# Optimization experiments

Hardware: AMD Instinct MI355X
Metric: run time of the kernel (lower is better)

## Reference

```python
import jax, jax.numpy as jnp
import numpy as np

B, SPLIT, D = 4096, 32, 256
UNITS = 256  # must equal D for the final view in the original module


def setup_inputs() -> dict:
    key = jax.random.key(0)
    kx, kw, kb = jax.random.split(key, 3)
    x = jax.random.normal(kx, (B, SPLIT, D), dtype=jnp.float32)
    W = jax.random.normal(kw, (SPLIT, D, UNITS), dtype=jnp.float32) * 0.02
    b = jax.random.normal(kb, (SPLIT, UNITS), dtype=jnp.float32) * 0.02
    return {"x": x, "W": W, "b": b}


def reference(x, W, b):
    # Original: loop over split dim, per-split matmul + bias + activation, concat,
    # then view(B, split, input_dim). Fused here as a single batched einsum.
    out = jnp.einsum('bsd,sdu->bsu', x, W) + b[None, :, :]
    out = jax.nn.relu(out)  # activation
    # concat along dim 1 then view(B, split, input_dim) == [B, SPLIT, UNITS] since UNITS == D
    return out
```

## Files before the change

### kernel.cpp

```cpp
#include <hip/hip_runtime.h>
#include <hip/hip_bf16.h>

typedef __attribute__((ext_vector_type(8))) short bf16x8;
typedef __attribute__((ext_vector_type(4))) float f32x4;

#define SPLITN 32
#define DDIM   256
#define UNITS  256
#define BROWS  4096

#define NIT  16
#define MCHN (BROWS / (NIT * 16))

static __device__ __forceinline__ ushort f2bf(float f) {
    __hip_bfloat16 h = __float2bfloat16(f);
    return *reinterpret_cast<ushort*>(&h);
}

static __device__ __forceinline__ bf16x8 cvt8(f32x4 lo, f32x4 hi) {
    union { uint u32[4]; bf16x8 v; } r;
    r.u32[0] = (uint)f2bf(lo[0]) | ((uint)f2bf(lo[1]) << 16);
    r.u32[1] = (uint)f2bf(lo[2]) | ((uint)f2bf(lo[3]) << 16);
    r.u32[2] = (uint)f2bf(hi[0]) | ((uint)f2bf(hi[1]) << 16);
    r.u32[3] = (uint)f2bf(hi[2]) | ((uint)f2bf(hi[3]) << 16);
    return r.v;
}

__global__ __launch_bounds__(256) void wt_prep(const float* __restrict__ W,
                                               ushort* __restrict__ Wt) {
    __shared__ float tile[64][65];
    const int s  = blockIdx.z;
    const int d0 = blockIdx.y * 64;
    const int u0 = blockIdx.x * 64;
    const int t  = threadIdx.x;

    const float* Ws = W + s * 65536;
    #pragma unroll
    for (int i = 0; i < 4; ++i) {
        int f  = t + i * 256;
        int d  = f >> 4;
        int uq = f & 15;
        f32x4 v = *reinterpret_cast<const f32x4*>(Ws + (d0 + d) * 256 + u0 + uq * 4);
        tile[d][uq * 4 + 0] = v[0];
        tile[d][uq * 4 + 1] = v[1];
        tile[d][uq * 4 + 2] = v[2];
        tile[d][uq * 4 + 3] = v[3];
    }
    __syncthreads();

    ushort* Wts = Wt + s * 65536;
    #pragma unroll
    for (int i = 0; i < 4; ++i) {
        int g  = t + i * 256;
        int u  = g >> 4;
        int dq = g & 15;
        uint lo = (uint)f2bf(tile[dq * 4 + 0][u]) | ((uint)f2bf(tile[dq * 4 + 1][u]) << 16);
        uint hi = (uint)f2bf(tile[dq * 4 + 2][u]) | ((uint)f2bf(tile[dq * 4 + 3][u]) << 16);
        uint2 val; val.x = lo; val.y = hi;
        *reinterpret_cast<uint2*>(Wts + (u0 + u) * 256 + d0 + dq * 4) = val;
    }
}

__global__ __launch_bounds__(256, 2) void lc_gemm(const float* __restrict__ x,
                                                  const ushort* __restrict__ Wt,
                                                  const float* __restrict__ bias,
                                                  float* __restrict__ out) {
    const int bid = blockIdx.x;
    const int sw  = (bid & 7) * 64 + (bid >> 3);
    const int s   = sw >> 4;
    const int mc  = sw & 15;
    const int m0  = mc * (NIT * 16);

    const int t  = threadIdx.x;
    const int wc = t >> 6;
    const int l  = t & 63;
    const int lr = l & 15;
    const int lg = l >> 4;

    bf16x8 Bf[4][8];
    {
        const ushort* wb = Wt + s * 65536 + (wc * 64 + lr) * 256 + lg * 8;
        #pragma unroll
        for (int ni = 0; ni < 4; ++ni)
            #pragma unroll
            for (int k = 0; k < 8; ++k)
                Bf[ni][k] = *reinterpret_cast<const bf16x8*>(wb + ni * (16 * 256) + k * 32);
    }

    float bv[4];
    #pragma unroll
    for (int ni = 0; ni < 4; ++ni)
        bv[ni] = bias[s * 256 + wc * 64 + ni * 16 + lr];

    const float* xp = x + (long)(m0 + lr) * 8192 + s * 256 + lg * 8;

    f32x4 a[8][2];
    #pragma unroll
    for (int k = 0; k < 8; ++k) {
        a[k][0] = *reinterpret_cast<const f32x4*>(xp + k * 32);
        a[k][1] = *reinterpret_cast<const f32x4*>(xp + k * 32 + 4);
    }

    float* op = out + (long)(m0 + lg * 4) * 8192 + s * 256 + wc * 64 + lr;

    for (int it = 0; it < NIT; ++it) {
        const int nit = (it + 1 < NIT) ? (it + 1) : it;
        const float* xn = xp + (long)nit * (16 * 8192);

        f32x4 acc[4];
        #pragma unroll
        for (int ni = 0; ni < 4; ++ni) {
            f32x4 z = {0.f, 0.f, 0.f, 0.f};
            acc[ni] = z;
        }

        #pragma unroll
        for (int k = 0; k < 8; ++k) {
            bf16x8 af = cvt8(a[k][0], a[k][1]);
            f32x4 n0 = *reinterpret_cast<const f32x4*>(xn + k * 32);
            f32x4 n1 = *reinterpret_cast<const f32x4*>(xn + k * 32 + 4);
            #pragma unroll
            for (int ni = 0; ni < 4; ++ni)
                acc[ni] = __builtin_amdgcn_mfma_f32_16x16x32_bf16(
                    af, Bf[ni][k], acc[ni], 0, 0, 0);
            a[k][0] = n0;
            a[k][1] = n1;
        }

        #pragma unroll
        for (int ni = 0; ni < 4; ++ni) {
            #pragma unroll
            for (int rr = 0; rr < 4; ++rr) {
                float v = fmaxf(acc[ni][rr] + bv[ni], 0.f);
                __builtin_nontemporal_store(
                    v, op + (long)(it * 16 + rr) * 8192 + ni * 16);
            }
        }
    }
}

__global__ void naive_lc(const float* __restrict__ x, const float* __restrict__ W,
                         const float* __restrict__ b, float* __restrict__ out,
                         int total) {
    int i = blockIdx.x * blockDim.x + threadIdx.x;
    if (i >= total) return;
    int u = i & 255;
    int s = (i >> 8) & 31;
    int bi = i >> 13;
    const float* xr = x + (long)bi * 8192 + s * 256;
    const float* wc = W + s * 65536 + u;
    float acc = 0.f;
    #pragma unroll 4
    for (int d = 0; d < 256; ++d) acc += xr[d] * wc[d * 256];
    out[i] = fmaxf(acc + b[s * 256 + u], 0.f);
}

extern "C" void kernel_launch(void* const* d_in, const int* in_sizes, int n_in,
                              void* d_out, int out_size, void* d_ws, size_t ws_size,
                              hipStream_t stream) {
    const float* x = (const float*)d_in[0];
    const float* W = (const float*)d_in[1];
    const float* b = (const float*)d_in[2];
    float* out = (float*)d_out;

    const size_t wt_bytes = (size_t)SPLITN * DDIM * UNITS * sizeof(ushort);
    if (ws_size >= wt_bytes) {
        ushort* Wt = (ushort*)d_ws;
        wt_prep<<<dim3(4, 4, 32), 256, 0, stream>>>(W, Wt);
        lc_gemm<<<dim3(SPLITN * MCHN), 256, 0, stream>>>(x, Wt, b, out);
    } else {
        int total = BROWS * SPLITN * UNITS;
        naive_lc<<<(total + 255) / 256, 256, 0, stream>>>(x, W, b, out, total);
    }
}
```

Baseline: 270.1 us.

## Swap operand residency: keep x fragments in registers, stream weights per column chunk

```diff
diff --git a/kernel.cpp b/kernel.cpp
--- a/kernel.cpp
+++ b/kernel.cpp
@@ -8,9 +8,6 @@
 #define DDIM   256
 #define UNITS  256
 #define BROWS  4096
-
-#define NIT  16
-#define MCHN (BROWS / (NIT * 16))
 
 static __device__ __forceinline__ ushort f2bf(float f) {
     __hip_bfloat16 h = __float2bfloat16(f);
@@ -61,51 +58,38 @@
     }
 }
 
-__global__ __launch_bounds__(256, 2) void lc_gemm(const float* __restrict__ x,
+__global__ __launch_bounds__(256, 5) void lc_gemm(const float* __restrict__ x,
                                                   const ushort* __restrict__ Wt,
                                                   const float* __restrict__ bias,
                                                   float* __restrict__ out) {
     const int bid = blockIdx.x;
-    const int sw  = (bid & 7) * 64 + (bid >> 3);
-    const int s   = sw >> 4;
-    const int mc  = sw & 15;
-    const int m0  = mc * (NIT * 16);
+    const int sw  = (bid & 7) * 256 + (bid >> 3);
+    const int s   = sw >> 6;
+    const int rc  = sw & 63;
+    const int t   = threadIdx.x;
+    const int w   = t >> 6, l = t & 63;
+    const int lr  = l & 15, lg = l >> 4;
+    const int m0  = rc * 64 + w * 16;
 
-    const int t  = threadIdx.x;
-    const int wc = t >> 6;
-    const int l  = t & 63;
-    const int lr = l & 15;
-    const int lg = l >> 4;
-
-    bf16x8 Bf[4][8];
-    {
-        const ushort* wb = Wt + s * 65536 + (wc * 64 + lr) * 256 + lg * 8;
-        #pragma unroll
-        for (int ni = 0; ni < 4; ++ni)
-            #pragma unroll
-            for (int k = 0; k < 8; ++k)
-                Bf[ni][k] = *reinterpret_cast<const bf16x8*>(wb + ni * (16 * 256) + k * 32);
+    const float* xp = x + (long)(m0 + lr) * 8192 + s * 256 + lg * 8;
+    bf16x8 Af[8];
+    #pragma unroll
+    for (int k = 0; k < 8; ++k) {
+        f32x4 lo = *reinterpret_cast<const f32x4*>(xp + k * 32);
+        f32x4 hi = *reinterpret_cast<const f32x4*>(xp + k * 32 + 4);
+        Af[k] = cvt8(lo, hi);
     }
 
-    float bv[4];
-    #pragma unroll
-    for (int ni = 0; ni < 4; ++ni)
-        bv[ni] = bias[s * 256 + wc * 64 + ni * 16 + lr];
+    const ushort* wb = Wt + s * 65536 + lr * 256 + lg * 8;
+    const float*  bb = bias + s * 256 + lr;
+    float*        ob = out + (long)(m0 + lg * 4) * 8192 + s * 256 + lr;
 
-    const float* xp = x + (long)(m0 + lr) * 8192 + s * 256 + lg * 8;
+    for (int c = 0; c < 4; ++c) {
+        const ushort* wbc = wb + c * (64 * 256);
 
-    f32x4 a[8][2];
-    #pragma unroll
-    for (int k = 0; k < 8; ++k) {
-        a[k][0] = *reinterpret_cast<const f32x4*>(xp + k * 32);
-        a[k][1] = *reinterpret_cast<const f32x4*>(xp + k * 32 + 4);
-    }
-
-    float* op = out + (long)(m0 + lg * 4) * 8192 + s * 256 + wc * 64 + lr;
-
-    for (int it = 0; it < NIT; ++it) {
-        const int nit = (it + 1 < NIT) ? (it + 1) : it;
-        const float* xn = xp + (long)nit * (16 * 8192);
+        float bv[4];
+        #pragma unroll
+        for (int ni = 0; ni < 4; ++ni) bv[ni] = bb[c * 64 + ni * 16];
 
         f32x4 acc[4];
         #pragma unroll
@@ -114,28 +98,38 @@
             acc[ni] = z;
         }
 
+        bf16x8 B0[4], B1[4];
         #pragma unroll
-        for (int k = 0; k < 8; ++k) {
-            bf16x8 af = cvt8(a[k][0], a[k][1]);
-            f32x4 n0 = *reinterpret_cast<const f32x4*>(xn + k * 32);
-            f32x4 n1 = *reinterpret_cast<const f32x4*>(xn + k * 32 + 4);
+        for (int ni = 0; ni < 4; ++ni)
+            B0[ni] = *reinterpret_cast<const bf16x8*>(wbc + ni * (16 * 256));
+
+        #pragma unroll
+        for (int k = 0; k < 8; k += 2) {
+            #pragma unroll
+            for (int ni = 0; ni < 4; ++ni)
+                B1[ni] = *reinterpret_cast<const bf16x8*>(wbc + ni * (16 * 256) + (k + 1) * 32);
             #pragma unroll
             for (int ni = 0; ni < 4; ++ni)
                 acc[ni] = __builtin_amdgcn_mfma_f32_16x16x32_bf16(
-                    af, Bf[ni][k], acc[ni], 0, 0, 0);
-            a[k][0] = n0;
-            a[k][1] = n1;
+                    Af[k], B0[ni], acc[ni], 0, 0, 0);
+            if (k + 2 < 8) {
+                #pragma unroll
+                for (int ni = 0; ni < 4; ++ni)
+                    B0[ni] = *reinterpret_cast<const bf16x8*>(wbc + ni * (16 * 256) + (k + 2) * 32);
+            }
+            #pragma unroll
+            for (int ni = 0; ni < 4; ++ni)
+                acc[ni] = __builtin_amdgcn_mfma_f32_16x16x32_bf16(
+                    Af[k + 1], B1[ni], acc[ni], 0, 0, 0);
         }
 
         #pragma unroll
-        for (int ni = 0; ni < 4; ++ni) {
+        for (int ni = 0; ni < 4; ++ni)
             #pragma unroll
             for (int rr = 0; rr < 4; ++rr) {
                 float v = fmaxf(acc[ni][rr] + bv[ni], 0.f);
-                __builtin_nontemporal_store(
-                    v, op + (long)(it * 16 + rr) * 8192 + ni * 16);
+                ob[(long)rr * 8192 + c * 64 + ni * 16] = v;
             }
-        }
     }
 }
 
@@ -167,7 +161,7 @@
     if (ws_size >= wt_bytes) {
         ushort* Wt = (ushort*)d_ws;
         wt_prep<<<dim3(4, 4, 32), 256, 0, stream>>>(W, Wt);
-        lc_gemm<<<dim3(SPLITN * MCHN), 256, 0, stream>>>(x, Wt, b, out);
+        lc_gemm<<<dim3(2048), 256, 0, stream>>>(x, Wt, b, out);
     } else {
         int total = BROWS * SPLITN * UNITS;
         naive_lc<<<(total + 255) / 256, 256, 0, stream>>>(x, W, b, out, total);
```

Measured after the change: 384.5 us. +42.4%, slower.
